# Kernel optimization log

Measured on AMD Instinct MI355X. Metric: run time of the kernel, lower is better.

## Reference

```python
import jax, jax.numpy as jnp
import numpy as np

D = 1024   # n_embd
H = 16     # n_head
NL = 6     # n_layer
B = 16
L = 64
T = 3 * L  # interleaved (rtg, state, action) tokens
NB = 100   # rtg bucket number
DF = 4 * D


def _ln(x, g, b, eps=1e-5):
    mu = jnp.mean(x, -1, keepdims=True)
    var = jnp.mean((x - mu) ** 2, -1, keepdims=True)
    return (x - mu) * jax.lax.rsqrt(var + eps) * g + b


def _gelu(x):
    return jax.nn.gelu(x, approximate=False)  # matches torch F.gelu (erf)


def setup_inputs() -> dict:
    key = jax.random.key(0)
    ks = iter(jax.random.split(key, 64))
    def rn(shape, s=0.02):
        return jax.random.normal(next(ks), shape, jnp.float32) * s
    inp = dict(
        states=jax.random.normal(next(ks), (B, L, 91), jnp.float32),
        actions=jax.random.normal(next(ks), (B, L, 1, 27), jnp.float32),
        rtgs=jax.random.uniform(next(ks), (B, L), jnp.float32) * 100.0,
        attention_mask=jnp.ones((B, L), bool),
        y_len=L,
        # state encoder: Linear(91,D) GELU Linear(D,D) GELU
        se_w1=rn((91, D)), se_b1=jnp.zeros(D), se_w2=rn((D, D)), se_b2=jnp.zeros(D),
        # action encoder: Linear(27,D) GELU Linear(D,D)
        ae_w1=rn((27, D)), ae_b1=jnp.zeros(D), ae_w2=rn((D, D)), ae_b2=jnp.zeros(D),
        # Autodis
        ad_bucket_w=rn((1, D)), ad_bucket_b=jnp.zeros(D), ad_ret_w=rn((1, NB)), ad_res_w=rn((NB, NB)),
        pos_emb=rn((1, T, D)),
        # transformer blocks (stacked over layers)
        ln1_g=jnp.ones((NL, D)), ln1_b=jnp.zeros((NL, D)),
        Wq=rn((NL, D, D)), bq=jnp.zeros((NL, D)),
        Wk=rn((NL, D, D)), bk=jnp.zeros((NL, D)),
        Wv=rn((NL, D, D)), bv=jnp.zeros((NL, D)),
        Wp=rn((NL, D, D)), bp=jnp.zeros((NL, D)),
        ln2_g=jnp.ones((NL, D)), ln2_b=jnp.zeros((NL, D)),
        Wm1=rn((NL, D, DF)), bm1=jnp.zeros((NL, DF)),
        Wm2=rn((NL, DF, D)), bm2=jnp.zeros((NL, D)),
        lin_w=rn((D, 27)), lin_b=jnp.zeros(27),
    )
    return inp


def _forward(attention_mask, states, actions, rtgs, se_w1, se_b1, se_w2, se_b2,
             ae_w1, ae_b1, ae_w2, ae_b2, ad_bucket_w, ad_bucket_b, ad_ret_w, ad_res_w,
             pos_emb, ln1_g, ln1_b, Wq, bq, Wk, bk, Wv, bv, Wp, bp,
             ln2_g, ln2_b, Wm1, bm1, Wm2, bm2, lin_w, lin_b):
    Bsz, Ls = states.shape[0], states.shape[1]
    Ts = 3 * Ls
    hd = D // H
    # encoders
    state_emb = _gelu(_gelu(states @ se_w1 + se_b1) @ se_w2 + se_b2)          # [B,L,D]
    act = actions[:, :, 0, :]                                                  # squeeze(2) -> [B,L,27]
    action_emb = _gelu(act @ ae_w1 + ae_b1) @ ae_w2 + ae_b2                    # [B,L,D]
    # Autodis rtg embedding
    bucket_value = jnp.linspace(0.0, 100.0, NB).reshape(NB, 1)
    meta = bucket_value @ ad_bucket_w + ad_bucket_b                            # [NB,D]
    s = jax.nn.leaky_relu(rtgs[..., None] @ ad_ret_w)                          # [B,L,NB]
    s = s + s @ ad_res_w
    e = jnp.exp(s - jnp.max(s, -1, keepdims=True))
    p = e / (1e-8 + jnp.sum(e, -1, keepdims=True))
    rtg_emb = p @ meta                                                         # [B,L,D]
    # interleave rtg/state/action tokens -> [B,3L,D]
    tok = jnp.stack([rtg_emb, state_emb, action_emb], axis=2).reshape(Bsz, Ts, D)
    x = tok + pos_emb[:, :Ts]
    # combined padding + causal mask
    m = jnp.repeat(attention_mask, 3, axis=1)                                  # [B,3L]
    causal = jnp.tril(jnp.ones((Ts, Ts), bool))
    fmask = m[:, None, :, None] & m[:, None, None, :] & causal[None, None]     # [B,1,T,T]
    scale = 1.0 / np.sqrt(hd)
    for i in range(NL):
        h = _ln(x, ln1_g[i], ln1_b[i])
        q = (h @ Wq[i] + bq[i]).reshape(Bsz, Ts, H, hd).transpose(0, 2, 1, 3)
        k = (h @ Wk[i] + bk[i]).reshape(Bsz, Ts, H, hd).transpose(0, 2, 1, 3)
        v = (h @ Wv[i] + bv[i]).reshape(Bsz, Ts, H, hd).transpose(0, 2, 1, 3)
        att = jnp.einsum('bhid,bhjd->bhij', q, k) * scale
        att = jnp.where(fmask, att, -1e9)
        att = jax.nn.softmax(att, axis=-1)
        y = jnp.einsum('bhij,bhjd->bhid', att, v).transpose(0, 2, 1, 3).reshape(Bsz, Ts, D)
        x = x + (y @ Wp[i] + bp[i])
        h2 = _ln(x, ln2_g[i], ln2_b[i])
        x = x + _gelu(h2 @ Wm1[i] + bm1[i]) @ Wm2[i] + bm2[i]
    return x @ lin_w + lin_b                                                   # [B,3L,27]


def reference(states, actions, rtgs, attention_mask, y_len, se_w1, se_b1, se_w2, se_b2,
              ae_w1, ae_b1, ae_w2, ae_b2, ad_bucket_w, ad_bucket_b, ad_ret_w, ad_res_w,
              pos_emb, ln1_g, ln1_b, Wq, bq, Wk, bk, Wv, bv, Wp, bp,
              ln2_g, ln2_b, Wm1, bm1, Wm2, bm2, lin_w, lin_b):
    return _forward(attention_mask, states, actions, rtgs, se_w1, se_b1, se_w2, se_b2,
                    ae_w1, ae_b1, ae_w2, ae_b2, ad_bucket_w, ad_bucket_b, ad_ret_w, ad_res_w,
                    pos_emb, ln1_g, ln1_b, Wq, bq, Wk, bk, Wv, bv, Wp, bp,
                    ln2_g, ln2_b, Wm1, bm1, Wm2, bm2, lin_w, lin_b)
```

## Files before the change

kernel.cpp:

```cpp
#include <hip/hip_runtime.h>
#include <cmath>

typedef unsigned short u16;
typedef unsigned int   u32;
typedef short s16x8 __attribute__((ext_vector_type(8)));
typedef float f32x4 __attribute__((ext_vector_type(4)));

#define D_  1024
#define H_  16
#define NL_ 6
#define B_  16
#define L_  64
#define T_  192
#define NB_ 100
#define DF_ 4096
#define BT_ (B_*T_)
#define BL_ (B_*L_)

__device__ __forceinline__ float b2f(u16 u){ u32 x = ((u32)u)<<16; return __uint_as_float(x); }
__device__ __forceinline__ u16 f2b(float f){ u32 x = __float_as_uint(f); x += 0x7fffu + ((x>>16)&1u); return (u16)(x>>16); }
__device__ __forceinline__ float gelu_f(float v){ return 0.5f*v*(1.0f+erff(v*0.70710678118f)); }

typedef const unsigned int __attribute__((address_space(1)))* as1_u32p;
typedef unsigned int __attribute__((address_space(3)))* as3_u32p;
__device__ __forceinline__ void gload16(const void* g, void* l)
{
    __builtin_amdgcn_global_load_lds((as1_u32p)g, (as3_u32p)l, 16, 0, 0);
}

__device__ __forceinline__ void tconv_tile(const float* __restrict__ W,
                                           u16* __restrict__ Wt,
                                           int K, int N, int nb, int kb, int tid)
{
    __shared__ float tile[64][65];
    int tr = tid >> 4, tc = tid & 15;
#pragma unroll
    for (int rr = 0; rr < 4; ++rr) {
        int k = tr + rr*16;
        float4 v = *(const float4*)(W + (size_t)(kb + k)*N + nb + tc*4);
        tile[k][tc*4+0] = v.x; tile[k][tc*4+1] = v.y;
        tile[k][tc*4+2] = v.z; tile[k][tc*4+3] = v.w;
    }
    __syncthreads();
#pragma unroll
    for (int rr = 0; rr < 4; ++rr) {
        int n = tr + rr*16;
        ushort4 o;
        o.x = f2b(tile[tc*4+0][n]);
        o.y = f2b(tile[tc*4+1][n]);
        o.z = f2b(tile[tc*4+2][n]);
        o.w = f2b(tile[tc*4+3][n]);
        *(ushort4*)(Wt + (size_t)(nb + n)*K + kb + tc*4) = o;
    }
}

__global__ __launch_bounds__(256) void tconv_kernel(const float* __restrict__ W,
                                                    u16* __restrict__ Wt,
                                                    int K, int N)
{
    tconv_tile(W, Wt, K, N, blockIdx.x*64, blockIdx.y*64, threadIdx.x);
}

__global__ __launch_bounds__(256) void tconv4L_kernel(const float* __restrict__ Wq,
                                                      const float* __restrict__ Wk,
                                                      const float* __restrict__ Wv,
                                                      const float* __restrict__ Wp,
                                                      u16* __restrict__ Wqkvt,
                                                      u16* __restrict__ Wpt,
                                                      int layer)
{
    int sel = blockIdx.z;
    size_t DD = (size_t)D_*D_;
    const float* Wz = ((sel == 0) ? Wq : (sel == 1) ? Wk : (sel == 2) ? Wv : Wp) + layer*DD;
    u16* Wtz = (sel == 3) ? (Wpt + layer*DD) : (Wqkvt + layer*3*DD + sel*DD);
    tconv_tile(Wz, Wtz, D_, D_, blockIdx.x*64, blockIdx.y*64, threadIdx.x);
}

__global__ __launch_bounds__(256) void tconv_mlpL_kernel(const float* __restrict__ Wm1,
                                                         const float* __restrict__ Wm2,
                                                         u16* __restrict__ Wm1t,
                                                         u16* __restrict__ Wm2t,
                                                         int layer)
{
    size_t DDF = (size_t)D_*DF_;
    int t = blockIdx.x;
    if (t < 1024) {
        int nbi = t & 63, kbi = t >> 6;
        tconv_tile(Wm1 + layer*DDF, Wm1t + layer*DDF, D_, DF_, nbi*64, kbi*64, threadIdx.x);
    } else {
        int t2 = t - 1024;
        int nbi = t2 & 15, kbi = t2 >> 4;
        tconv_tile(Wm2 + layer*DDF, Wm2t + layer*DDF, DF_, D_, nbi*64, kbi*64, threadIdx.x);
    }
}

__global__ __launch_bounds__(256) void pack_qkv_bias_kernel(const float* __restrict__ bq,
                                                            const float* __restrict__ bk,
                                                            const float* __restrict__ bv,
                                                            float* __restrict__ out)
{
    int i = blockIdx.x*256 + threadIdx.x;
    int layer = i / 3072;
    int r = i - layer*3072;
    int c = r >> 10, d = r & 1023;
    const float* src = (c == 0) ? bq : (c == 1) ? bk : bv;
    out[i] = src[layer*1024 + d];
}

__global__ __launch_bounds__(256) void tlin_kernel(const float* __restrict__ w,
                                                   float* __restrict__ wt)
{
    int k = blockIdx.x*256 + threadIdx.x;
#pragma unroll 1
    for (int c = 0; c < 27; ++c)
        wt[c*1024 + k] = w[k*27 + c];
}

__global__ __launch_bounds__(256) void embed1_kernel(const float* __restrict__ A,
                                                     const float* __restrict__ W,
                                                     const float* __restrict__ bias,
                                                     u16* __restrict__ out, int K)
{
    int idx = blockIdx.x*256 + threadIdx.x;
    int m = idx >> 10, n = idx & 1023;
    float acc = bias[n];
    for (int k = 0; k < K; ++k)
        acc += A[m*K + k] * W[k*1024 + n];
    out[idx] = f2b(gelu_f(acc));
}

__global__ __launch_bounds__(128) void rtg_kernel(const float* __restrict__ rtgs,
                                                  const float* __restrict__ ret_w,
                                                  const float* __restrict__ res_w,
                                                  const float* __restrict__ bucket_w,
                                                  const float* __restrict__ bucket_b,
                                                  float* __restrict__ eR)
{
    int r = blockIdx.x, tid = threadIdx.x;
    __shared__ float sarr[NB_];
    __shared__ float red[128];
    float rtg = rtgs[r];
    float s = 0.f;
    if (tid < NB_) {
        float v = rtg * ret_w[tid];
        s = (v > 0.f) ? v : 0.01f*v;
        sarr[tid] = s;
    }
    __syncthreads();
    float s2 = -1e30f;
    if (tid < NB_) {
        float acc = s;
        for (int m = 0; m < NB_; ++m) acc += sarr[m] * res_w[m*NB_ + tid];
        s2 = acc;
    }
    red[tid] = s2; __syncthreads();
    for (int off = 64; off > 0; off >>= 1) { if (tid < off) red[tid] = fmaxf(red[tid], red[tid+off]); __syncthreads(); }
    float mx = red[0]; __syncthreads();
    float e = (tid < NB_) ? expf(s2 - mx) : 0.f;
    red[tid] = e; __syncthreads();
    for (int off = 64; off > 0; off >>= 1) { if (tid < off) red[tid] += red[tid+off]; __syncthreads(); }
    float S = red[0]; __syncthreads();
    float bv = (100.f/99.f) * (float)tid;
    red[tid] = e * bv; __syncthreads();
    for (int off = 64; off > 0; off >>= 1) { if (tid < off) red[tid] += red[tid+off]; __syncthreads(); }
    float EB = red[0];
    float inv = 1.f/(1e-8f + S);
    float c = EB * inv, sg = S * inv;
    for (int d = tid; d < D_; d += 128)
        eR[(size_t)r*D_ + d] = c*bucket_w[d] + sg*bucket_b[d];
}

__global__ __launch_bounds__(256) void assemble_kernel(const float* __restrict__ eR,
                                                       const float* __restrict__ eS,
                                                       const float* __restrict__ eA,
                                                       const float* __restrict__ pos,
                                                       float* __restrict__ xf)
{
    int idx = blockIdx.x*256 + threadIdx.x;
    int row = idx >> 10, d = idx & 1023;
    int b = row / T_, t = row % T_;
    int l = t / 3, c = t % 3;
    const float* src = (c == 0) ? eR : (c == 1) ? eS : eA;
    xf[idx] = src[(size_t)(b*L_ + l)*D_ + d] + pos[(size_t)t*D_ + d];
}

template<int NP>
__global__ __launch_bounds__(256) void ln_kernel(const float* __restrict__ x,
                                                 const float* __restrict__ parts,
                                                 size_t pstride,
                                                 const float* __restrict__ g,
                                                 const float* __restrict__ bb,
                                                 float* __restrict__ xout,
                                                 u16* __restrict__ out)
{
    int row = blockIdx.x*4 + (threadIdx.x >> 6);
    int lane = threadIdx.x & 63;
    const float4* xr = (const float4*)(x + (size_t)row*D_);
    float4 v[4];
    float s = 0.f, q = 0.f;
#pragma unroll
    for (int i = 0; i < 4; ++i) {
        float4 a = xr[lane + i*64];
        if (NP == 4) {
#pragma unroll
            for (int z = 0; z < 4; ++z) {
                float4 p = ((const float4*)(parts + (size_t)z*pstride + (size_t)row*D_))[lane + i*64];
                a.x += p.x; a.y += p.y; a.z += p.z; a.w += p.w;
            }
        }
        v[i] = a;
        s += a.x+a.y+a.z+a.w;
        q += a.x*a.x+a.y*a.y+a.z*a.z+a.w*a.w;
    }
    if (NP == 4) {
#pragma unroll
        for (int i = 0; i < 4; ++i)
            ((float4*)(xout + (size_t)row*D_))[lane + i*64] = v[i];
    }
#pragma unroll
    for (int off = 1; off < 64; off <<= 1) {
        s += __shfl_xor(s, off, 64);
        q += __shfl_xor(q, off, 64);
    }
    float mean = s*(1.f/(float)D_);
    float var  = q*(1.f/(float)D_) - mean*mean;
    float rstd = rsqrtf(var + 1e-5f);
#pragma unroll
    for (int i = 0; i < 4; ++i) {
        int d0 = (lane + i*64)*4;
        ushort4 ov;
        ov.x = f2b((v[i].x-mean)*rstd*g[d0+0] + bb[d0+0]);
        ov.y = f2b((v[i].y-mean)*rstd*g[d0+1] + bb[d0+1]);
        ov.z = f2b((v[i].z-mean)*rstd*g[d0+2] + bb[d0+2]);
        ov.w = f2b((v[i].w-mean)*rstd*g[d0+3] + bb[d0+3]);
        ((ushort4*)(out + (size_t)row*D_))[lane + i*64] = ov;
    }
}

template<int GELU_ACT, int SPLITK, int ATOMIC>
__global__ __launch_bounds__(256) void gemm_bt(const u16* __restrict__ A,
                                               const u16* __restrict__ Bt,
                                               const float* __restrict__ bias,
                                               float* __restrict__ outF,
                                               u16* __restrict__ outB,
                                               int M, int N, int K, int kc,
                                               size_t partStride)
{
    __shared__ __align__(16) u16 As[3*128*32];
    __shared__ __align__(16) u16 Bs[3*128*32];
    int tid = threadIdx.x;

    int gx = gridDim.x;
    int nwg = gx * gridDim.y;
    int id = blockIdx.y * gx + blockIdx.x;
    int q8 = nwg >> 3;
    int nid = (id & 7) * q8 + (id >> 3);
    int n0 = (nid % gx) * 128;
    int m0 = (nid / gx) * 128;

    int wave = tid >> 6, lane = tid & 63;
    int wm = (wave >> 1) * 64, wn = (wave & 1) * 64;
    int lr = lane & 15, lq = lane >> 4;
    int slotRd = (lq ^ ((lr >> 1) & 3)) * 8;

    int srow = tid >> 2;
    int sslot = (tid & 3) ^ ((srow >> 1) & 3);

    int k0 = (SPLITK > 1) ? blockIdx.z * kc : 0;
    int nIt = ((SPLITK > 1) ? kc : K) >> 5;

    const u16* ap0 = A  + (size_t)(m0 + srow) * K + k0 + sslot * 8;
    const u16* ap1 = ap0 + (size_t)64 * K;
    const u16* bp0 = Bt + (size_t)(n0 + srow) * K + k0 + sslot * 8;
    const u16* bp1 = bp0 + (size_t)64 * K;

    u16 *sA0 = As, *sA1 = As + 4096, *sA2 = As + 8192;
    u16 *sB0 = Bs, *sB1 = Bs + 4096, *sB2 = Bs + 8192;
    int woff = wave * 512;

    f32x4 acc[4][4];
#pragma unroll
    for (int i = 0; i < 4; ++i)
#pragma unroll
        for (int j = 0; j < 4; ++j) acc[i][j] = (f32x4){0.f,0.f,0.f,0.f};

    gload16(ap0, sA0 + woff); gload16(ap1, sA0 + 2048 + woff);
    gload16(bp0, sB0 + woff); gload16(bp1, sB0 + 2048 + woff);
    ap0 += 32; ap1 += 32; bp0 += 32; bp1 += 32;
    gload16(ap0, sA1 + woff); gload16(ap1, sA1 + 2048 + woff);
    gload16(bp0, sB1 + woff); gload16(bp1, sB1 + 2048 + woff);
    ap0 += 32; ap1 += 32; bp0 += 32; bp1 += 32;

    for (int it = 0; it < nIt; ++it) {
        if (it + 1 < nIt) asm volatile("s_waitcnt vmcnt(4)" ::: "memory");
        else              asm volatile("s_waitcnt vmcnt(0)" ::: "memory");
        asm volatile("s_barrier" ::: "memory");
        if (it + 2 < nIt) {
            gload16(ap0, sA2 + woff); gload16(ap1, sA2 + 2048 + woff);
            gload16(bp0, sB2 + woff); gload16(bp1, sB2 + 2048 + woff);
            ap0 += 32; ap1 += 32; bp0 += 32; bp1 += 32;
        }
        s16x8 af[4], bf[4];
#pragma unroll
        for (int i = 0; i < 4; ++i)
            af[i] = *(const s16x8*)(sA0 + (wm + i*16 + lr)*32 + slotRd);
#pragma unroll
        for (int j = 0; j < 4; ++j)
            bf[j] = *(const s16x8*)(sB0 + (wn + j*16 + lr)*32 + slotRd);
#pragma unroll
        for (int i = 0; i < 4; ++i)
#pragma unroll
            for (int j = 0; j < 4; ++j)
                acc[i][j] = __builtin_amdgcn_mfma_f32_16x16x32_bf16(af[i], bf[j], acc[i][j], 0, 0, 0);
        u16* t0 = sA0; sA0 = sA1; sA1 = sA2; sA2 = t0;
        u16* t1 = sB0; sB0 = sB1; sB1 = sB2; sB2 = t1;
    }

    float* outZ = (SPLITK > 1 && !ATOMIC) ? outF + (size_t)blockIdx.z * partStride : outF;
#pragma unroll
    for (int i = 0; i < 4; ++i) {
        int mbase = m0 + wm + i*16 + lq*4;
#pragma unroll
        for (int j = 0; j < 4; ++j) {
            int n = n0 + wn + j*16 + lr;
            float bvl = (SPLITK > 1) ? ((blockIdx.z == 0) ? bias[n] : 0.f) : bias[n];
#pragma unroll
            for (int r = 0; r < 4; ++r) {
                int m = mbase + r;
                float v = acc[i][j][r] + bvl;
                size_t off = (size_t)m*N + n;
                if (SPLITK > 1) {
                    if (ATOMIC) atomicAdd(outF + off, v);
                    else        outZ[off] = v;
                } else {
                    if (GELU_ACT) v = gelu_f(v);
                    if (outF) outF[off] = v;
                    if (outB) outB[off] = f2b(v);
                }
            }
        }
    }
}

__global__ __launch_bounds__(256) void attn_mfma_kernel(const u16* __restrict__ qkv,
                                                        u16* __restrict__ yb)
{
    __shared__ __align__(16) u16 Ks[192*72];
    __shared__ __align__(16) u16 Vt[64*200];
    __shared__ __align__(16) u16 Pch[4][16*40];

    int tid = threadIdx.x;
    int b = blockIdx.x >> 4, h = blockIdx.x & 15;
    int c = blockIdx.y;
    int nrows = (c + 1) * 64;
    int bT = b * T_;
    int colBase = h * 64;
    int w = tid >> 6, lane = tid & 63;
    int lr = lane & 15, lq = lane >> 4;
    const int S3 = 3 * D_;

    for (int it = 0; it < (nrows >> 5); ++it) {
        int cc = it*256 + tid;
        int row = cc >> 3, ch = cc & 7;
        *(int4*)(Ks + row*72 + ch*8) =
            *(const int4*)(qkv + (size_t)(bT+row)*S3 + D_ + colBase + ch*8);
        union { int4 v; u16 s[8]; } rv;
        rv.v = *(const int4*)(qkv + (size_t)(bT+row)*S3 + 2*D_ + colBase + ch*8);
#pragma unroll
        for (int i2 = 0; i2 < 8; ++i2)
            Vt[(ch*8 + i2)*200 + row] = rv.s[i2];
    }
    __syncthreads();

    u16* Ch = Pch[w];
    int qt = c*4 + w;
    int tqb = qt * 16;

    const u16* qrow = qkv + (size_t)(bT + tqb + lr)*S3 + colBase + lq*8;
    s16x8 af0 = *(const s16x8*)(qrow);
    s16x8 af1 = *(const s16x8*)(qrow + 32);

    f32x4 sacc[12];
#pragma unroll
    for (int jt = 0; jt < 12; ++jt) {
        if (jt <= qt) {
            s16x8 bk0 = *(const s16x8*)(Ks + (jt*16 + lr)*72 + lq*8);
            s16x8 bk1 = *(const s16x8*)(Ks + (jt*16 + lr)*72 + 32 + lq*8);
            f32x4 a = (f32x4){0.f,0.f,0.f,0.f};
            a = __builtin_amdgcn_mfma_f32_16x16x32_bf16(af0, bk0, a, 0, 0, 0);
            a = __builtin_amdgcn_mfma_f32_16x16x32_bf16(af1, bk1, a, 0, 0, 0);
            sacc[jt] = a;
        }
    }

    float mrow[4] = {-1e30f,-1e30f,-1e30f,-1e30f};
#pragma unroll
    for (int jt = 0; jt < 12; ++jt) if (jt <= qt) {
#pragma unroll
        for (int r = 0; r < 4; ++r) {
            bool valid = (jt < qt) || (lr <= lq*4 + r);
            float s = valid ? sacc[jt][r]*0.125f : -1e30f;
            sacc[jt][r] = s;
            mrow[r] = fmaxf(mrow[r], s);
        }
    }
#pragma unroll
    for (int r = 0; r < 4; ++r) {
#pragma unroll
        for (int off = 1; off < 16; off <<= 1)
            mrow[r] = fmaxf(mrow[r], __shfl_xor(mrow[r], off, 64));
    }

    float lrow[4] = {0.f,0.f,0.f,0.f};
#pragma unroll
    for (int jt = 0; jt < 12; ++jt) if (jt <= qt) {
#pragma unroll
        for (int r = 0; r < 4; ++r) {
            float e = __expf(sacc[jt][r] - mrow[r]);
            sacc[jt][r] = e;
            lrow[r] += e;
        }
    }
#pragma unroll
    for (int r = 0; r < 4; ++r) {
#pragma unroll
        for (int off = 1; off < 16; off <<= 1)
            lrow[r] += __shfl_xor(lrow[r], off, 64);
        lrow[r] = 1.f / lrow[r];
    }

    int nkt = (qt + 2) >> 1;
    f32x4 oacc[4];
#pragma unroll
    for (int nt = 0; nt < 4; ++nt) oacc[nt] = (f32x4){0.f,0.f,0.f,0.f};

#pragma unroll
    for (int kt = 0; kt < 6; ++kt) if (kt < nkt) {
        int jt0 = 2*kt, jt1 = 2*kt + 1;
#pragma unroll
        for (int r = 0; r < 4; ++r) {
            u16 e0 = f2b(sacc[jt0][r]);
            u16 e1 = (jt1 <= qt) ? f2b(sacc[jt1][r]) : (u16)0;
            Ch[(lq*4 + r)*40 + lr]      = e0;
            Ch[(lq*4 + r)*40 + 16 + lr] = e1;
        }
        s16x8 ap = *(const s16x8*)(Ch + lr*40 + lq*8);
#pragma unroll
        for (int nt = 0; nt < 4; ++nt) {
            s16x8 bv = *(const s16x8*)(Vt + (nt*16 + lr)*200 + kt*32 + lq*8);
            oacc[nt] = __builtin_amdgcn_mfma_f32_16x16x32_bf16(ap, bv, oacc[nt], 0, 0, 0);
        }
    }

#pragma unroll
    for (int nt = 0; nt < 4; ++nt)
#pragma unroll
        for (int r = 0; r < 4; ++r)
            yb[(size_t)(bT + tqb + lq*4 + r)*D_ + colBase + nt*16 + lr] =
                f2b(oacc[nt][r] * lrow[r]);
}

template<int NP>
__global__ __launch_bounds__(256) void final_kernel(const float* __restrict__ xf,
                                                    const float* __restrict__ parts,
                                                    size_t pstride,
                                                    const float* __restrict__ lin_wT,
                                                    const float* __restrict__ lin_b,
                                                    float* __restrict__ out)
{
    int row = blockIdx.x*4 + (threadIdx.x >> 6);
    int lane = threadIdx.x & 63;
    const float4* xr = (const float4*)(xf + (size_t)row*D_);
    float4 x[4];
#pragma unroll
    for (int i = 0; i < 4; ++i) {
        float4 v = xr[lane + i*64];
        if (NP == 4) {
#pragma unroll
            for (int z = 0; z < 4; ++z) {
                float4 p = ((const float4*)(parts + (size_t)z*pstride + (size_t)row*D_))[lane + i*64];
                v.x += p.x; v.y += p.y; v.z += p.z; v.w += p.w;
            }
        }
        x[i] = v;
    }
#pragma unroll 1
    for (int c = 0; c < 27; ++c) {
        const float4* wr = (const float4*)(lin_wT + (size_t)c*D_);
        float a = 0.f;
#pragma unroll
        for (int i = 0; i < 4; ++i) {
            float4 wv = wr[lane + i*64];
            a += x[i].x*wv.x + x[i].y*wv.y + x[i].z*wv.z + x[i].w*wv.w;
        }
#pragma unroll
        for (int off = 1; off < 64; off <<= 1)
            a += __shfl_xor(a, off, 64);
        if (lane == 0) out[(size_t)row*27 + c] = a + lin_b[c];
    }
}

extern "C" void kernel_launch(void* const* d_in, const int* in_sizes, int n_in,
                              void* d_out, int out_size, void* d_ws, size_t ws_size,
                              hipStream_t stream)
{
    const float* states   = (const float*)d_in[0];
    const float* actions  = (const float*)d_in[1];
    const float* rtgs     = (const float*)d_in[2];
    const float* se_w1 = (const float*)d_in[5];
    const float* se_b1 = (const float*)d_in[6];
    const float* se_w2 = (const float*)d_in[7];
    const float* se_b2 = (const float*)d_in[8];
    const float* ae_w1 = (const float*)d_in[9];
    const float* ae_b1 = (const float*)d_in[10];
    const float* ae_w2 = (const float*)d_in[11];
    const float* ae_b2 = (const float*)d_in[12];
    const float* ad_bucket_w = (const float*)d_in[13];
    const float* ad_bucket_b = (const float*)d_in[14];
    const float* ad_ret_w = (const float*)d_in[15];
    const float* ad_res_w = (const float*)d_in[16];
    const float* pos_emb  = (const float*)d_in[17];
    const float* ln1_g = (const float*)d_in[18];
    const float* ln1_b = (const float*)d_in[19];
    const float* Wq = (const float*)d_in[20];
    const float* bq = (const float*)d_in[21];
    const float* Wk = (const float*)d_in[22];
    const float* bk = (const float*)d_in[23];
    const float* Wv = (const float*)d_in[24];
    const float* bv = (const float*)d_in[25];
    const float* Wp = (const float*)d_in[26];
    const float* bp = (const float*)d_in[27];
    const float* ln2_g = (const float*)d_in[28];
    const float* ln2_b = (const float*)d_in[29];
    const float* Wm1 = (const float*)d_in[30];
    const float* bm1 = (const float*)d_in[31];
    const float* Wm2 = (const float*)d_in[32];
    const float* bm2 = (const float*)d_in[33];
    const float* lin_w = (const float*)d_in[34];
    const float* lin_b = (const float*)d_in[35];

    char* w = (char*)d_ws;
    auto take = [&](size_t bytes) { char* p = w; w += (bytes + 255) & ~(size_t)255; return p; };

    float* xf   = (float*)take((size_t)BT_*D_*4);
    u16* hb     = (u16*)take((size_t)BT_*D_*2);
    u16* qkvb   = (u16*)take((size_t)BT_*3*D_*2);
    char* scr   =        take((size_t)BT_*DF_*2);
    u16*  midb  = (u16*)scr;
    u16*  tSb   = (u16*)scr;
    u16*  tAb   = (u16*)(scr + (size_t)BL_*D_*2);
    float* eS   = (float*)(scr + (size_t)2*BL_*D_*2);
    float* eA   = (float*)(scr + (size_t)2*BL_*D_*2 + (size_t)BL_*D_*4);
    float* eR   = (float*)(scr + (size_t)2*BL_*D_*2 + (size_t)2*BL_*D_*4);
    float* pp   = (float*)take((size_t)4*BT_*D_*4);
    float* mq   = (float*)take((size_t)4*BT_*D_*4);

    u16* Wqkvt = (u16*)take((size_t)NL_*3*D_*D_*2);
    u16* Wpt   = (u16*)take((size_t)NL_*D_*D_*2);
    u16* Wm1t  = (u16*)take((size_t)NL_*D_*DF_*2);
    u16* Wm2t  = (u16*)take((size_t)NL_*DF_*D_*2);
    u16* sw2t  = (u16*)take((size_t)D_*D_*2);
    u16* aw2t  = (u16*)take((size_t)D_*D_*2);
    float* bqkv= (float*)take((size_t)NL_*3*D_*4);
    float* lwT = (float*)take((size_t)27*D_*4);

    size_t ask = (size_t)(w - (char*)d_ws);
    bool bigWS = (ws_size >= ask);

    const size_t PSTRIDE = (size_t)BT_*D_;
    size_t DD = (size_t)D_*D_, DDF = (size_t)D_*DF_;

    pack_qkv_bias_kernel<<<72, 256, 0, stream>>>(bq, bk, bv, bqkv);
    tlin_kernel<<<4, 256, 0, stream>>>(lin_w, lwT);
    tconv_kernel<<<dim3(16,16), 256, 0, stream>>>(se_w2, sw2t, D_, D_);
    tconv_kernel<<<dim3(16,16), 256, 0, stream>>>(ae_w2, aw2t, D_, D_);
    tconv4L_kernel<<<dim3(16,16,4), 256, 0, stream>>>(Wq, Wk, Wv, Wp, Wqkvt, Wpt, 0);
    tconv_mlpL_kernel<<<2048, 256, 0, stream>>>(Wm1, Wm2, Wm1t, Wm2t, 0);

    embed1_kernel<<<4096, 256, 0, stream>>>(states,  se_w1, se_b1, tSb, 91);
    embed1_kernel<<<4096, 256, 0, stream>>>(actions, ae_w1, ae_b1, tAb, 27);
    gemm_bt<1,1,0><<<dim3(8,8), 256, 0, stream>>>(tSb, sw2t, se_b2, eS, nullptr, BL_, D_, D_, D_, 0);
    gemm_bt<0,1,0><<<dim3(8,8), 256, 0, stream>>>(tAb, aw2t, ae_b2, eA, nullptr, BL_, D_, D_, D_, 0);
    rtg_kernel<<<BL_, 128, 0, stream>>>(rtgs, ad_ret_w, ad_res_w, ad_bucket_w, ad_bucket_b, eR);
    assemble_kernel<<<(BT_*D_)/256, 256, 0, stream>>>(eR, eS, eA, pos_emb, xf);

    for (int i = 0; i < NL_; ++i) {
        if (i > 0 && bigWS)
            ln_kernel<4><<<BT_/4, 256, 0, stream>>>(xf, mq, PSTRIDE, ln1_g + i*D_, ln1_b + i*D_, xf, hb);
        else
            ln_kernel<0><<<BT_/4, 256, 0, stream>>>(xf, nullptr, 0, ln1_g + i*D_, ln1_b + i*D_, nullptr, hb);
        gemm_bt<0,1,0><<<dim3(24,24), 256, 0, stream>>>(hb, Wqkvt + (size_t)i*3*DD, bqkv + i*3*D_,
                                                        nullptr, qkvb, BT_, 3*D_, D_, D_, 0);
        attn_mfma_kernel<<<dim3(B_*H_,3), 256, 0, stream>>>(qkvb, hb);
        if (i + 1 < NL_)
            tconv4L_kernel<<<dim3(16,16,4), 256, 0, stream>>>(Wq, Wk, Wv, Wp, Wqkvt, Wpt, i+1);
        if (bigWS)
            gemm_bt<0,4,0><<<dim3(8,24,4), 256, 0, stream>>>(hb, Wpt + (size_t)i*DD, bp + i*D_,
                                                             pp, nullptr, BT_, D_, D_, 256, PSTRIDE);
        else
            gemm_bt<0,2,1><<<dim3(8,24,2), 256, 0, stream>>>(hb, Wpt + (size_t)i*DD, bp + i*D_,
                                                             xf, nullptr, BT_, D_, D_, 512, 0);
        if (bigWS)
            ln_kernel<4><<<BT_/4, 256, 0, stream>>>(xf, pp, PSTRIDE, ln2_g + i*D_, ln2_b + i*D_, xf, hb);
        else
            ln_kernel<0><<<BT_/4, 256, 0, stream>>>(xf, nullptr, 0, ln2_g + i*D_, ln2_b + i*D_, nullptr, hb);
        gemm_bt<1,1,0><<<dim3(32,24), 256, 0, stream>>>(hb, Wm1t + (size_t)i*DDF, bm1 + i*DF_,
                                                        nullptr, midb, BT_, DF_, D_, D_, 0);
        if (bigWS)
            gemm_bt<0,4,0><<<dim3(8,24,4), 256, 0, stream>>>(midb, Wm2t + (size_t)i*DDF, bm2 + i*D_,
                                                             mq, nullptr, BT_, D_, DF_, 1024, PSTRIDE);
        else
            gemm_bt<0,2,1><<<dim3(8,24,2), 256, 0, stream>>>(midb, Wm2t + (size_t)i*DDF, bm2 + i*D_,
                                                             xf, nullptr, BT_, D_, DF_, 2048, 0);
        if (i + 1 < NL_)
            tconv_mlpL_kernel<<<2048, 256, 0, stream>>>(Wm1, Wm2, Wm1t, Wm2t, i+1);
    }

    if (bigWS)
        final_kernel<4><<<BT_/4, 256, 0, stream>>>(xf, mq, PSTRIDE, lwT, lin_b, (float*)d_out);
    else
        final_kernel<0><<<BT_/4, 256, 0, stream>>>(xf, nullptr, 0, lwT, lin_b, (float*)d_out);
}
```

Measured before the change: 1.534 ms.

## Fuse residual into proj GEMM, merge weight conversions, load K directly in attention

The attention output projection now runs as a single non-split GEMM that adds the residual in its epilogue and writes xf in place. This removes the split-K partial buffer and the partial-sum reduction in the second layernorm. The per-layer weight transpose/convert kernels for QKV/proj and MLP are merged into one launch issued after attention. The attention kernel no longer stages K in shared memory and instead reads K fragments directly from global memory, moving the barrier later. The risks are fewer workgroups for the projection GEMM (192 instead of 768) and uncoalesced K reads from global memory.

```diff
diff --git a/kernel.cpp b/kernel.cpp
--- a/kernel.cpp
+++ b/kernel.cpp
@@ -61,36 +61,31 @@
     tconv_tile(W, Wt, K, N, blockIdx.x*64, blockIdx.y*64, threadIdx.x);
 }
 
-__global__ __launch_bounds__(256) void tconv4L_kernel(const float* __restrict__ Wq,
-                                                      const float* __restrict__ Wk,
-                                                      const float* __restrict__ Wv,
-                                                      const float* __restrict__ Wp,
-                                                      u16* __restrict__ Wqkvt,
-                                                      u16* __restrict__ Wpt,
-                                                      int layer)
-{
-    int sel = blockIdx.z;
-    size_t DD = (size_t)D_*D_;
-    const float* Wz = ((sel == 0) ? Wq : (sel == 1) ? Wk : (sel == 2) ? Wv : Wp) + layer*DD;
-    u16* Wtz = (sel == 3) ? (Wpt + layer*DD) : (Wqkvt + layer*3*DD + sel*DD);
-    tconv_tile(Wz, Wtz, D_, D_, blockIdx.x*64, blockIdx.y*64, threadIdx.x);
-}
-
-__global__ __launch_bounds__(256) void tconv_mlpL_kernel(const float* __restrict__ Wm1,
-                                                         const float* __restrict__ Wm2,
-                                                         u16* __restrict__ Wm1t,
-                                                         u16* __restrict__ Wm2t,
-                                                         int layer)
-{
-    size_t DDF = (size_t)D_*DF_;
+__global__ __launch_bounds__(256) void tconvL_kernel(const float* __restrict__ Wq,
+                                                     const float* __restrict__ Wk,
+                                                     const float* __restrict__ Wv,
+                                                     const float* __restrict__ Wp,
+                                                     const float* __restrict__ Wm1,
+                                                     const float* __restrict__ Wm2,
+                                                     u16* __restrict__ Wqkvt,
+                                                     u16* __restrict__ Wpt,
+                                                     u16* __restrict__ Wm1t,
+                                                     u16* __restrict__ Wm2t,
+                                                     int layer)
+{
+    size_t DD = (size_t)D_*D_, DDF = (size_t)D_*DF_;
     int t = blockIdx.x;
     if (t < 1024) {
-        int nbi = t & 63, kbi = t >> 6;
-        tconv_tile(Wm1 + layer*DDF, Wm1t + layer*DDF, D_, DF_, nbi*64, kbi*64, threadIdx.x);
+        int sel = t >> 8, tt = t & 255;
+        const float* Wz = ((sel == 0) ? Wq : (sel == 1) ? Wk : (sel == 2) ? Wv : Wp) + layer*DD;
+        u16* Wtz = (sel == 3) ? (Wpt + layer*DD) : (Wqkvt + layer*3*DD + sel*DD);
+        tconv_tile(Wz, Wtz, D_, D_, (tt & 15)*64, (tt >> 4)*64, threadIdx.x);
+    } else if (t < 2048) {
+        int t2 = t - 1024;
+        tconv_tile(Wm1 + layer*DDF, Wm1t + layer*DDF, D_, DF_, (t2 & 63)*64, (t2 >> 6)*64, threadIdx.x);
     } else {
-        int t2 = t - 1024;
-        int nbi = t2 & 15, kbi = t2 >> 4;
-        tconv_tile(Wm2 + layer*DDF, Wm2t + layer*DDF, DF_, D_, nbi*64, kbi*64, threadIdx.x);
+        int t2 = t - 2048;
+        tconv_tile(Wm2 + layer*DDF, Wm2t + layer*DDF, DF_, D_, (t2 & 15)*64, (t2 >> 4)*64, threadIdx.x);
     }
 }
 
@@ -237,10 +232,11 @@
     }
 }
 
-template<int GELU_ACT, int SPLITK, int ATOMIC>
+template<int GELU_ACT, int SPLITK, int ATOMIC, int RES>
 __global__ __launch_bounds__(256) void gemm_bt(const u16* __restrict__ A,
                                                const u16* __restrict__ Bt,
                                                const float* __restrict__ bias,
+                                               const float* __restrict__ res,
                                                float* __restrict__ outF,
                                                u16* __restrict__ outB,
                                                int M, int N, int K, int kc,
@@ -334,6 +330,7 @@
                     else        outZ[off] = v;
                 } else {
                     if (GELU_ACT) v = gelu_f(v);
+                    if (RES)      v += res[off];
                     if (outF) outF[off] = v;
                     if (outB) outB[off] = f2b(v);
                 }
@@ -345,7 +342,6 @@
 __global__ __launch_bounds__(256) void attn_mfma_kernel(const u16* __restrict__ qkv,
                                                         u16* __restrict__ yb)
 {
-    __shared__ __align__(16) u16 Ks[192*72];
     __shared__ __align__(16) u16 Vt[64*200];
     __shared__ __align__(16) u16 Pch[4][16*40];
 
@@ -362,15 +358,12 @@
     for (int it = 0; it < (nrows >> 5); ++it) {
         int cc = it*256 + tid;
         int row = cc >> 3, ch = cc & 7;
-        *(int4*)(Ks + row*72 + ch*8) =
-            *(const int4*)(qkv + (size_t)(bT+row)*S3 + D_ + colBase + ch*8);
         union { int4 v; u16 s[8]; } rv;
         rv.v = *(const int4*)(qkv + (size_t)(bT+row)*S3 + 2*D_ + colBase + ch*8);
 #pragma unroll
         for (int i2 = 0; i2 < 8; ++i2)
             Vt[(ch*8 + i2)*200 + row] = rv.s[i2];
     }
-    __syncthreads();
 
     u16* Ch = Pch[w];
     int qt = c*4 + w;
@@ -384,8 +377,9 @@
 #pragma unroll
     for (int jt = 0; jt < 12; ++jt) {
         if (jt <= qt) {
-            s16x8 bk0 = *(const s16x8*)(Ks + (jt*16 + lr)*72 + lq*8);
-            s16x8 bk1 = *(const s16x8*)(Ks + (jt*16 + lr)*72 + 32 + lq*8);
+            const u16* kr = qkv + (size_t)(bT + jt*16 + lr)*S3 + D_ + colBase + lq*8;
+            s16x8 bk0 = *(const s16x8*)(kr);
+            s16x8 bk1 = *(const s16x8*)(kr + 32);
             f32x4 a = (f32x4){0.f,0.f,0.f,0.f};
             a = __builtin_amdgcn_mfma_f32_16x16x32_bf16(af0, bk0, a, 0, 0, 0);
             a = __builtin_amdgcn_mfma_f32_16x16x32_bf16(af1, bk1, a, 0, 0, 0);
@@ -428,6 +422,8 @@
             lrow[r] += __shfl_xor(lrow[r], off, 64);
         lrow[r] = 1.f / lrow[r];
     }
+
+    __syncthreads();
 
     int nkt = (qt + 2) >> 1;
     f32x4 oacc[4];
@@ -552,7 +548,6 @@
     float* eS   = (float*)(scr + (size_t)2*BL_*D_*2);
     float* eA   = (float*)(scr + (size_t)2*BL_*D_*2 + (size_t)BL_*D_*4);
     float* eR   = (float*)(scr + (size_t)2*BL_*D_*2 + (size_t)2*BL_*D_*4);
-    float* pp   = (float*)take((size_t)4*BT_*D_*4);
     float* mq   = (float*)take((size_t)4*BT_*D_*4);
 
     u16* Wqkvt = (u16*)take((size_t)NL_*3*D_*D_*2);
@@ -574,13 +569,13 @@
     tlin_kernel<<<4, 256, 0, stream>>>(lin_w, lwT);
     tconv_kernel<<<dim3(16,16), 256, 0, stream>>>(se_w2, sw2t, D_, D_);
     tconv_kernel<<<dim3(16,16), 256, 0, stream>>>(ae_w2, aw2t, D_, D_);
-    tconv4L_kernel<<<dim3(16,16,4), 256, 0, stream>>>(Wq, Wk, Wv, Wp, Wqkvt, Wpt, 0);
-    tconv_mlpL_kernel<<<2048, 256, 0, stream>>>(Wm1, Wm2, Wm1t, Wm2t, 0);
+    tconvL_kernel<<<3072, 256, 0, stream>>>(Wq, Wk, Wv, Wp, Wm1, Wm2,
+                                            Wqkvt, Wpt, Wm1t, Wm2t, 0);
 
     embed1_kernel<<<4096, 256, 0, stream>>>(states,  se_w1, se_b1, tSb, 91);
     embed1_kernel<<<4096, 256, 0, stream>>>(actions, ae_w1, ae_b1, tAb, 27);
-    gemm_bt<1,1,0><<<dim3(8,8), 256, 0, stream>>>(tSb, sw2t, se_b2, eS, nullptr, BL_, D_, D_, D_, 0);
-    gemm_bt<0,1,0><<<dim3(8,8), 256, 0, stream>>>(tAb, aw2t, ae_b2, eA, nullptr, BL_, D_, D_, D_, 0);
+    gemm_bt<1,1,0,0><<<dim3(8,8), 256, 0, stream>>>(tSb, sw2t, se_b2, nullptr, eS, nullptr, BL_, D_, D_, D_, 0);
+    gemm_bt<0,1,0,0><<<dim3(8,8), 256, 0, stream>>>(tAb, aw2t, ae_b2, nullptr, eA, nullptr, BL_, D_, D_, D_, 0);
     rtg_kernel<<<BL_, 128, 0, stream>>>(rtgs, ad_ret_w, ad_res_w, ad_bucket_w, ad_bucket_b, eR);
     assemble_kernel<<<(BT_*D_)/256, 256, 0, stream>>>(eR, eS, eA, pos_emb, xf);
 
@@ -589,31 +584,23 @@
             ln_kernel<4><<<BT_/4, 256, 0, stream>>>(xf, mq, PSTRIDE, ln1_g + i*D_, ln1_b + i*D_, xf, hb);
         else
             ln_kernel<0><<<BT_/4, 256, 0, stream>>>(xf, nullptr, 0, ln1_g + i*D_, ln1_b + i*D_, nullptr, hb);
-        gemm_bt<0,1,0><<<dim3(24,24), 256, 0, stream>>>(hb, Wqkvt + (size_t)i*3*DD, bqkv + i*3*D_,
-                                                        nullptr, qkvb, BT_, 3*D_, D_, D_, 0);
+        gemm_bt<0,1,0,0><<<dim3(24,24), 256, 0, stream>>>(hb, Wqkvt + (size_t)i*3*DD, bqkv + i*3*D_,
+                                                          nullptr, nullptr, qkvb, BT_, 3*D_, D_, D_, 0);
         attn_mfma_kernel<<<dim3(B_*H_,3), 256, 0, stream>>>(qkvb, hb);
         if (i + 1 < NL_)
-            tconv4L_kernel<<<dim3(16,16,4), 256, 0, stream>>>(Wq, Wk, Wv, Wp, Wqkvt, Wpt, i+1);
+            tconvL_kernel<<<3072, 256, 0, stream>>>(Wq, Wk, Wv, Wp, Wm1, Wm2,
+                                                    Wqkvt, Wpt, Wm1t, Wm2t, i+1);
+        gemm_bt<0,1,0,1><<<dim3(8,24), 256, 0, stream>>>(hb, Wpt + (size_t)i*DD, bp + i*D_,
+                                                         xf, xf, nullptr, BT_, D_, D_, D_, 0);
+        ln_kernel<0><<<BT_/4, 256, 0, stream>>>(xf, nullptr, 0, ln2_g + i*D_, ln2_b + i*D_, nullptr, hb);
+        gemm_bt<1,1,0,0><<<dim3(32,24), 256, 0, stream>>>(hb, Wm1t + (size_t)i*DDF, bm1 + i*DF_,
+                                                          nullptr, nullptr, midb, BT_, DF_, D_, D_, 0);
         if (bigWS)
-            gemm_bt<0,4,0><<<dim3(8,24,4), 256, 0, stream>>>(hb, Wpt + (size_t)i*DD, bp + i*D_,
-                                                             pp, nullptr, BT_, D_, D_, 256, PSTRIDE);
+            gemm_bt<0,4,0,0><<<dim3(8,24,4), 256, 0, stream>>>(midb, Wm2t + (size_t)i*DDF, bm2 + i*D_,
+                                                               nullptr, mq, nullptr, BT_, D_, DF_, 1024, PSTRIDE);
         else
-            gemm_bt<0,2,1><<<dim3(8,24,2), 256, 0, stream>>>(hb, Wpt + (size_t)i*DD, bp + i*D_,
-                                                             xf, nullptr, BT_, D_, D_, 512, 0);
-        if (bigWS)
-            ln_kernel<4><<<BT_/4, 256, 0, stream>>>(xf, pp, PSTRIDE, ln2_g + i*D_, ln2_b + i*D_, xf, hb);
-        else
-            ln_kernel<0><<<BT_/4, 256, 0, stream>>>(xf, nullptr, 0, ln2_g + i*D_, ln2_b + i*D_, nullptr, hb);
-        gemm_bt<1,1,0><<<dim3(32,24), 256, 0, stream>>>(hb, Wm1t + (size_t)i*DDF, bm1 + i*DF_,
-                                                        nullptr, midb, BT_, DF_, D_, D_, 0);
-        if (bigWS)
-            gemm_bt<0,4,0><<<dim3(8,24,4), 256, 0, stream>>>(midb, Wm2t + (size_t)i*DDF, bm2 + i*D_,
-                                                             mq, nullptr, BT_, D_, DF_, 1024, PSTRIDE);
-        else
-            gemm_bt<0,2,1><<<dim3(8,24,2), 256, 0, stream>>>(midb, Wm2t + (size_t)i*DDF, bm2 + i*D_,
-                                                             xf, nullptr, BT_, D_, DF_, 2048, 0);
-        if (i + 1 < NL_)
-            tconv_mlpL_kernel<<<2048, 256, 0, stream>>>(Wm1, Wm2, Wm1t, Wm2t, i+1);
+            gemm_bt<0,2,1,0><<<dim3(8,24,2), 256, 0, stream>>>(midb, Wm2t + (size_t)i*DDF, bm2 + i*D_,
+                                                               nullptr, xf, nullptr, BT_, D_, DF_, 2048, 0);
     }
 
     if (bigWS)
```

After: 1.603 ms. 4.5% more time.
